# Optimization experiments

Measured on AMD Instinct MI355X. Metric: run time of the kernel, lower is better.

The kernel has to match this reference:

```python
import jax, jax.numpy as jnp
import numpy as np

B, D, L, H, HD, FF, WS, P = 64, 768, 12, 12, 64, 3072, 14, 16
N = WS * WS + 1  # 197 tokens (cls + 196 patches)
NRD = (2 * WS - 1) ** 2 + 3  # 732 relative distances
SCALE = HD ** -0.5


def _rel_index():
    coords = np.stack(np.meshgrid(np.arange(WS), np.arange(WS), indexing='ij')).reshape(2, -1)
    rel = (coords[:, :, None] - coords[:, None, :]).transpose(1, 2, 0)
    rel[..., 0] += WS - 1
    rel[..., 1] += WS - 1
    rel[..., 0] *= 2 * WS - 1
    idx = np.zeros((N, N), np.int32)
    idx[1:, 1:] = rel.sum(-1)
    idx[0, :] = NRD - 3
    idx[:, 0] = NRD - 2
    idx[0, 0] = NRD - 1
    return jnp.asarray(idx)

REL_IDX = _rel_index()


def setup_inputs() -> dict:
    key = jax.random.key(0)
    ks = jax.random.split(key, 12)
    rn = lambda k, shp: jax.random.normal(k, shp, jnp.float32) * 0.02
    return dict(
        x=jax.random.normal(ks[0], (B, 3, 224, 224), jnp.float32),
        patch_w=rn(ks[1], (D, 3 * P * P)),
        patch_b=jnp.zeros((D,), jnp.float32),
        cls_token=rn(ks[2], (1, 1, D)),
        pos_embed=rn(ks[3], (1, N, D)),
        ln1_w=jnp.ones((L, D), jnp.float32), ln1_b=jnp.zeros((L, D), jnp.float32),
        qkv_w=rn(ks[4], (L, 3 * D, D)),
        q_bias=jnp.zeros((L, D), jnp.float32), v_bias=jnp.zeros((L, D), jnp.float32),
        proj_w=rn(ks[5], (L, D, D)), proj_b=jnp.zeros((L, D), jnp.float32),
        ln2_w=jnp.ones((L, D), jnp.float32), ln2_b=jnp.zeros((L, D), jnp.float32),
        fc1_w=rn(ks[6], (L, FF, D)), fc1_b=jnp.zeros((L, FF), jnp.float32),
        fc2_w=rn(ks[7], (L, D, FF)), fc2_b=jnp.zeros((L, D), jnp.float32),
        gamma1=jnp.full((L, D), 0.1, jnp.float32), gamma2=jnp.full((L, D), 0.1, jnp.float32),
        rpb_table=rn(ks[8], (L, NRD, H)),
        fc_norm_w=jnp.ones((D,), jnp.float32), fc_norm_b=jnp.zeros((D,), jnp.float32),
    )


def _ln(x, w, b):
    mu = x.mean(-1, keepdims=True)
    var = ((x - mu) ** 2).mean(-1, keepdims=True)
    return (x - mu) * jax.lax.rsqrt(var + 1e-5) * w + b


def reference(x, patch_w, patch_b, cls_token, pos_embed, ln1_w, ln1_b, qkv_w, q_bias, v_bias,
              proj_w, proj_b, ln2_w, ln2_b, fc1_w, fc1_b, fc2_w, fc2_b, gamma1, gamma2,
              rpb_table, fc_norm_w, fc_norm_b):
    # Patch embed (Conv2d stride=kernel == patch extraction + matmul): [B,3,224,224] -> [B,196,D]
    p = x.reshape(B, 3, WS, P, WS, P).transpose(0, 2, 4, 1, 3, 5).reshape(B, WS * WS, 3 * P * P)
    t = p @ patch_w.T + patch_b
    t = jnp.concatenate([jnp.broadcast_to(cls_token, (B, 1, D)), t], axis=1) + pos_embed
    for l in range(L):
        h = _ln(t, ln1_w[l], ln1_b[l])
        qkvb = jnp.concatenate([q_bias[l], jnp.zeros((D,), t.dtype), v_bias[l]])
        qkv = (h @ qkv_w[l].T + qkvb).reshape(B, N, 3, H, HD).transpose(2, 0, 3, 1, 4)
        q, k, v = qkv[0] * SCALE, qkv[1], qkv[2]
        attn = jnp.einsum('bhnd,bhmd->bhnm', q, k)  # [B,H,N,N]
        bias = rpb_table[l][REL_IDX]  # [N,N,H] gathered relative-position bias
        attn = jax.nn.softmax(attn + bias.transpose(2, 0, 1)[None], axis=-1)
        o = jnp.einsum('bhnm,bhmd->bhnd', attn, v).transpose(0, 2, 1, 3).reshape(B, N, D)
        t = t + gamma1[l] * (o @ proj_w[l].T + proj_b[l])
        h = _ln(t, ln2_w[l], ln2_b[l])
        h = jax.nn.gelu(h @ fc1_w[l].T + fc1_b[l], approximate=False) @ fc2_w[l].T + fc2_b[l]
        t = t + gamma2[l] * h
    feat = t[:, 1:].mean(axis=1)  # mean-pool patch tokens (use_mean_pooling)
    return _ln(feat, fc_norm_w, fc_norm_b)
```

## Files before the change

### kernel.cpp

```cpp
#include <hip/hip_runtime.h>
#include <hip/hip_bf16.h>

typedef short bf16x8 __attribute__((ext_vector_type(8)));
typedef float f32x4 __attribute__((ext_vector_type(4)));

constexpr int D_  = 768;
constexpr int FF_ = 3072;
constexpr int HH  = 12;
constexpr int NT_ = 197;
constexpr int BB  = 64;
constexpr int BR  = BB * NT_;
constexpr int MP  = 12800;
constexpr int SN  = 224;
constexpr float SCALE_ = 0.125f;

#define MFMA16(a, b, c) __builtin_amdgcn_mfma_f32_16x16x32_bf16((a), (b), (c), 0, 0, 0)

__device__ __forceinline__ void gload_lds16(const __hip_bfloat16* g, __hip_bfloat16* l) {
  __builtin_amdgcn_global_load_lds((const __attribute__((address_space(1))) void*)g,
                                   (__attribute__((address_space(3))) void*)l, 16, 0, 0);
}


__global__ void patch_build(const float* __restrict__ x, __hip_bfloat16* __restrict__ p) {
  int e = blockIdx.x * 256 + threadIdx.x;
  int idx4 = e * 4;
  int col = idx4 % 768; int m = idx4 / 768;
  int c = col >> 8; int pi = (col >> 4) & 15; int pj = col & 15;
  int b = m / 196; int s = m - b * 196; int wi = s / 14; int wj = s - wi * 14;
  const float* src = x + (((size_t)b * 3 + c) * 224 + wi * 16 + pi) * 224 + wj * 16 + pj;
  float4 v = *(const float4*)src;
  __hip_bfloat16* dst = p + (size_t)idx4;
  dst[0] = __float2bfloat16(v.x);
  dst[1] = __float2bfloat16(v.y);
  dst[2] = __float2bfloat16(v.z);
  dst[3] = __float2bfloat16(v.w);
}

__global__ void cls_pos(const float* __restrict__ cls_tok, const float* __restrict__ pos, __hip_bfloat16* __restrict__ t) {
  int e = blockIdx.x * 256 + threadIdx.x;
  int b = e / 768, c = e - (e / 768) * 768;
  t[(size_t)(b * NT_) * D_ + c] = __float2bfloat16(cls_tok[c] + pos[c]);
}

__global__ void cvt_bf16(const float* __restrict__ in, __hip_bfloat16* __restrict__ out) {
  int e = blockIdx.x * 256 + threadIdx.x;
  float4 v = ((const float4*)in)[e];
  union { __hip_bfloat16 h[4]; short4 s4; } u;
  u.h[0] = __float2bfloat16(v.x); u.h[1] = __float2bfloat16(v.y);
  u.h[2] = __float2bfloat16(v.z); u.h[3] = __float2bfloat16(v.w);
  ((short4*)out)[e] = u.s4;
}

__global__ void cvt_layer(const float* __restrict__ qkv, const float* __restrict__ proj,
                          const float* __restrict__ fc1, const float* __restrict__ fc2,
                          __hip_bfloat16* __restrict__ wq, __hip_bfloat16* __restrict__ wp,
                          __hip_bfloat16* __restrict__ w1, __hip_bfloat16* __restrict__ w2) {
  int e = blockIdx.x * 256 + threadIdx.x;
  const float* src; __hip_bfloat16* dst;
  if (e < 442368)       { src = qkv; dst = wq; }
  else if (e < 589824)  { src = proj; dst = wp; e -= 442368; }
  else if (e < 1179648) { src = fc1;  dst = w1; e -= 589824; }
  else                  { src = fc2;  dst = w2; e -= 1179648; }
  float4 v = ((const float4*)src)[e];
  union { __hip_bfloat16 h[4]; short4 s4; } u;
  u.h[0] = __float2bfloat16(v.x); u.h[1] = __float2bfloat16(v.y);
  u.h[2] = __float2bfloat16(v.z); u.h[3] = __float2bfloat16(v.w);
  ((short4*)dst)[e] = u.s4;
}

__global__ void build_bias(const float* __restrict__ rpb, __hip_bfloat16* __restrict__ bias_all) {
  int e = blockIdx.x * 256 + threadIdx.x;
  int j = e % SN; int rest = e / SN; int i = rest % SN; int l = rest / SN;
  int idx;
  if (i >= 197 || j >= 197) idx = 0;
  else if (i == 0 && j == 0) idx = 731;
  else if (i == 0) idx = 729;
  else if (j == 0) idx = 730;
  else {
    int pi = i - 1, pj = j - 1;
    int ri = pi / 14, ci = pi - ri * 14, rj = pj / 14, cj = pj - rj * 14;
    idx = (ri - rj + 13) * 27 + (ci - cj + 13);
  }
  const float* src = rpb + ((size_t)l * 732 + idx) * HH;
  __hip_bfloat16* dst = bias_all + ((size_t)l * HH * SN + i) * SN + j;
  #pragma unroll
  for (int h = 0; h < HH; ++h) dst[(size_t)h * SN * SN] = __float2bfloat16(src[h]);
}

__global__ __launch_bounds__(256) void transp_v(const __hip_bfloat16* __restrict__ vb,
                                                __hip_bfloat16* __restrict__ vtb) {
  int bh = blockIdx.x;
  __shared__ unsigned short V_lds[SN][65];
  const unsigned short* src = (const unsigned short*)(vb + (size_t)bh * SN * 64);
  unsigned short* dst = (unsigned short*)(vtb + (size_t)bh * 64 * SN);
  int tid = threadIdx.x;
  #pragma unroll
  for (int c = 0; c < 14; ++c) {
    int id = c * 256 + tid;
    int e = id * 4;
    int nn = e >> 6, d = e & 63;
    ushort4 v = ((const ushort4*)src)[id];
    V_lds[nn][d] = v.x; V_lds[nn][d + 1] = v.y; V_lds[nn][d + 2] = v.z; V_lds[nn][d + 3] = v.w;
  }
  __syncthreads();
  #pragma unroll
  for (int c = 0; c < 14; ++c) {
    int id = c * 256 + tid;
    int e = id * 4;
    int d = e / SN, nn = e - d * SN;
    ushort4 v;
    v.x = V_lds[nn][d]; v.y = V_lds[nn + 1][d]; v.z = V_lds[nn + 2][d]; v.w = V_lds[nn + 3][d];
    ((ushort4*)dst)[id] = v;
  }
}

__device__ __forceinline__ void block_reduce2(float& s, float& q, int tid) {
  #pragma unroll
  for (int d = 32; d >= 1; d >>= 1) { s += __shfl_xor(s, d); q += __shfl_xor(q, d); }
  __shared__ float ss[4], qq[4];
  int wave = tid >> 6, lane = tid & 63;
  if (lane == 0) { ss[wave] = s; qq[wave] = q; }
  __syncthreads();
  s = ss[0] + ss[1] + ss[2] + ss[3];
  q = qq[0] + qq[1] + qq[2] + qq[3];
}

__global__ __launch_bounds__(256) void ln_rows(const __hip_bfloat16* __restrict__ t, const float* __restrict__ w,
                                               const float* __restrict__ b, __hip_bfloat16* __restrict__ out) {
  int row = blockIdx.x; int tid = threadIdx.x;
  const __hip_bfloat16* x = t + (size_t)row * D_;
  float v0 = __bfloat162float(x[tid]);
  float v1 = __bfloat162float(x[tid + 256]);
  float v2 = __bfloat162float(x[tid + 512]);
  float s = v0 + v1 + v2;
  float q = v0 * v0 + v1 * v1 + v2 * v2;
  block_reduce2(s, q, tid);
  float mu = s * (1.0f / 768.0f);
  float var = q * (1.0f / 768.0f) - mu * mu;
  float rs = rsqrtf(var + 1e-5f);
  __hip_bfloat16* o = out + (size_t)row * D_;
  o[tid]       = __float2bfloat16((v0 - mu) * rs * w[tid]       + b[tid]);
  o[tid + 256] = __float2bfloat16((v1 - mu) * rs * w[tid + 256] + b[tid + 256]);
  o[tid + 512] = __float2bfloat16((v2 - mu) * rs * w[tid + 512] + b[tid + 512]);
}

__global__ __launch_bounds__(256) void pool_ln(const __hip_bfloat16* __restrict__ t, const float* __restrict__ w,
                                               const float* __restrict__ b, float* __restrict__ out) {
  int bimg = blockIdx.x; int tid = threadIdx.x;
  const __hip_bfloat16* base = t + ((size_t)bimg * NT_ + 1) * D_;
  float a0 = 0.f, a1 = 0.f, a2 = 0.f;
  for (int s = 0; s < 196; ++s) {
    const __hip_bfloat16* r = base + (size_t)s * D_;
    a0 += __bfloat162float(r[tid]);
    a1 += __bfloat162float(r[tid + 256]);
    a2 += __bfloat162float(r[tid + 512]);
  }
  a0 *= (1.0f / 196.0f); a1 *= (1.0f / 196.0f); a2 *= (1.0f / 196.0f);
  float s = a0 + a1 + a2;
  float q = a0 * a0 + a1 * a1 + a2 * a2;
  block_reduce2(s, q, tid);
  float mu = s * (1.0f / 768.0f);
  float var = q * (1.0f / 768.0f) - mu * mu;
  float rs = rsqrtf(var + 1e-5f);
  float* o = out + (size_t)bimg * D_;
  o[tid]       = (a0 - mu) * rs * w[tid]       + b[tid];
  o[tid + 256] = (a1 - mu) * rs * w[tid + 256] + b[tid + 256];
  o[tid + 512] = (a2 - mu) * rs * w[tid + 512] + b[tid + 512];
}


enum { EPI_PATCH = 0, EPI_QKV = 1, EPI_GELU = 2, EPI_RESID = 3 };

struct GemmArgs {
  const __hip_bfloat16* A;
  const __hip_bfloat16* W;
  int K;
  int NTILES;
  const float* bias;
  const float* bias2;
  const float* gamma;
  const float* pos;
  __hip_bfloat16* tout;
  __hip_bfloat16* out;
  __hip_bfloat16* qo;
  __hip_bfloat16* ko;
  __hip_bfloat16* vo;
};

template <int MODE, int BM_>
__device__ __forceinline__ void gemm_body(GemmArgs p) {
  static_assert(BM_ == 128 || BM_ == 64, "");
  constexpr int MREP = BM_ / 32;
  const int tid = threadIdx.x, lane = tid & 63, wave = tid >> 6;
  const int wr = wave >> 1, wc = wave & 1;
  const int l15 = lane & 15, l4 = lane >> 4;
  const int K = p.K;

  const int nwg = gridDim.x;
  const int q = nwg >> 3, rm = nwg & 7;
  const int xcd = blockIdx.x & 7, sub = blockIdx.x >> 3;
  const int swb = (xcd < rm ? xcd * (q + 1) : rm * (q + 1) + (xcd - rm) * q) + sub;
  const int bn = swb % p.NTILES, bm = swb / p.NTILES;

  __shared__ __align__(16) __hip_bfloat16 As[BM_ * 64];
  __shared__ __align__(16) __hip_bfloat16 Bs[128 * 64];

  const int sr = tid >> 3, sc = tid & 7;
  const int swz = (sc ^ (sr & 7)) * 8;
  const __hip_bfloat16* a0 = p.A + (size_t)(bm * BM_ + sr) * K + swz;
  const __hip_bfloat16* b0 = p.W + (size_t)(bn * 128 + sr) * K + swz;
  const int ldsoff = wave * 512;

  auto stage = [&](int t) {
    #pragma unroll
    for (int i = 0; i < BM_ / 32; ++i)
      gload_lds16(a0 + (size_t)(i * 32) * K + (size_t)t * 64, &As[i * 2048 + ldsoff]);
    #pragma unroll
    for (int i = 0; i < 4; ++i)
      gload_lds16(b0 + (size_t)(i * 32) * K + (size_t)t * 64, &Bs[i * 2048 + ldsoff]);
  };
  auto rdA = [&](int m, int ks) {
    int row = wr * (BM_ / 2) + m * 16 + l15;
    return *(const bf16x8*)&As[row * 64 + (((ks << 2) + l4) ^ (row & 7)) * 8];
  };
  auto rdB = [&](int n, int ks) {
    int row = wc * 64 + n * 16 + l15;
    return *(const bf16x8*)&Bs[row * 64 + (((ks << 2) + l4) ^ (row & 7)) * 8];
  };

  f32x4 acc[MREP][4] = {};
  const int NKT = K >> 6;
  for (int t = 0; t < NKT; ++t) {
    if (t) asm volatile("s_barrier" ::: "memory");
    stage(t);
    asm volatile("s_waitcnt vmcnt(0)" ::: "memory");
    asm volatile("s_barrier" ::: "memory");
    #pragma unroll
    for (int ks = 0; ks < 2; ++ks) {
      bf16x8 af[MREP], bfr[4];
      #pragma unroll
      for (int m = 0; m < MREP; ++m) af[m] = rdA(m, ks);
      #pragma unroll
      for (int n = 0; n < 4; ++n) bfr[n] = rdB(n, ks);
      #pragma unroll
      for (int m = 0; m < MREP; ++m)
        #pragma unroll
        for (int n = 0; n < 4; ++n)
          acc[m][n] = MFMA16(af[m], bfr[n], acc[m][n]);
    }
  }

  const int mb = bm * BM_ + wr * (BM_ / 2);
  const int nbase = bn * 128 + wc * 64;
  if constexpr (MODE == EPI_QKV) {
    #pragma unroll
    for (int j = 0; j < 4; ++j) {
      const int n = nbase + j * 16 + l15;
      const int which = n / D_, d = n - which * D_;
      const int head = d >> 6, hd = d & 63;
      #pragma unroll
      for (int i = 0; i < MREP; ++i) {
        #pragma unroll
        for (int rr = 0; rr < 4; ++rr) {
          const int m = mb + i * 16 + l4 * 4 + rr;
          if (m < BR) {
            const int b = m / NT_, nn = m - (m / NT_) * NT_;
            float v = acc[i][j][rr];
            if (which == 0)
              p.qo[(((size_t)(b * HH + head)) * SN + nn) * 64 + hd] = __float2bfloat16((v + p.bias[d]) * SCALE_);
            else if (which == 1)
              p.ko[(((size_t)(b * HH + head)) * SN + nn) * 64 + hd] = __float2bfloat16(v);
            else
              p.vo[(((size_t)(b * HH + head)) * SN + nn) * 64 + hd] = __float2bfloat16(v + p.bias2[d]);
          }
        }
      }
    }
  } else {
    #pragma unroll
    for (int i = 0; i < MREP; ++i) {
      #pragma unroll
      for (int rr = 0; rr < 4; ++rr) {
        const int m = mb + i * 16 + l4 * 4 + rr;
        if constexpr (MODE == EPI_PATCH) {
          const int b = m / 196, s = m - (m / 196) * 196;
          __hip_bfloat16* dst = p.tout + ((size_t)(b * NT_ + s + 1)) * D_;
          const float* pose = p.pos + (size_t)(s + 1) * D_;
          #pragma unroll
          for (int j = 0; j < 4; ++j) {
            int n = nbase + j * 16 + l15;
            dst[n] = __float2bfloat16(acc[i][j][rr] + p.bias[n] + pose[n]);
          }
        } else if constexpr (MODE == EPI_GELU) {
          __hip_bfloat16* dst = p.out + (size_t)m * FF_;
          #pragma unroll
          for (int j = 0; j < 4; ++j) {
            int n = nbase + j * 16 + l15;
            float u = acc[i][j][rr] + p.bias[n];
            float z = 1.59576912f * (u + 0.044715f * u * u * u);
            float g = u * (1.0f / (1.0f + __expf(-z)));
            dst[n] = __float2bfloat16(g);
          }
        } else {
          if (m < BR) {
            __hip_bfloat16* dst = p.tout + (size_t)m * D_;
            #pragma unroll
            for (int j = 0; j < 4; ++j) {
              int n = nbase + j * 16 + l15;
              float old = __bfloat162float(dst[n]);
              dst[n] = __float2bfloat16(old + p.gamma[n] * (acc[i][j][rr] + p.bias[n]));
            }
          }
        }
      }
    }
  }
}

__global__ __launch_bounds__(256, 4) void gA_patch(GemmArgs p) { gemm_body<EPI_PATCH, 128>(p); }
__global__ __launch_bounds__(256, 4) void gB_qkv(GemmArgs p)   { gemm_body<EPI_QKV, 128>(p); }
__global__ __launch_bounds__(256, 4) void gC_proj(GemmArgs p)  { gemm_body<EPI_RESID, 64>(p); }
__global__ __launch_bounds__(256, 4) void gD_fc1(GemmArgs p)   { gemm_body<EPI_GELU, 128>(p); }
__global__ __launch_bounds__(256, 4) void gE_fc2(GemmArgs p)   { gemm_body<EPI_RESID, 64>(p); }


__global__ __launch_bounds__(256) void attn_kernel(const __hip_bfloat16* __restrict__ qb,
    const __hip_bfloat16* __restrict__ kb, const __hip_bfloat16* __restrict__ vtb,
    const __hip_bfloat16* __restrict__ biasL, __hip_bfloat16* __restrict__ o) {
  int bh = blockIdx.x; int b = bh / HH, h = bh - b * HH;
  int lane = threadIdx.x & 63, wave = threadIdx.x >> 6;
  int l15 = lane & 15, l4 = lane >> 4;
  __shared__ __align__(16) __hip_bfloat16 probs[4][16][SN];
  const __hip_bfloat16* Q  = qb  + (size_t)bh * SN * 64;
  const __hip_bfloat16* Kp = kb  + (size_t)bh * SN * 64;
  const __hip_bfloat16* VT = vtb + (size_t)bh * 64 * SN;
  const __hip_bfloat16* BIAS = biasL + (size_t)h * SN * SN;
  for (int mt = wave; mt < 13; mt += 4) {
    int m0 = mt * 16;
    bf16x8 qf0 = *(const bf16x8*)(Q + ((size_t)(m0 + l15)) * 64 + l4 * 8);
    bf16x8 qf1 = *(const bf16x8*)(Q + ((size_t)(m0 + l15)) * 64 + 32 + l4 * 8);
    f32x4 sc[14] = {};
    #pragma unroll
    for (int nt = 0; nt < 14; ++nt) {
      bf16x8 kf0 = *(const bf16x8*)(Kp + ((size_t)(nt * 16 + l15)) * 64 + l4 * 8);
      bf16x8 kf1 = *(const bf16x8*)(Kp + ((size_t)(nt * 16 + l15)) * 64 + 32 + l4 * 8);
      sc[nt] = __builtin_amdgcn_mfma_f32_16x16x32_bf16(qf0, kf0, sc[nt], 0, 0, 0);
      sc[nt] = __builtin_amdgcn_mfma_f32_16x16x32_bf16(qf1, kf1, sc[nt], 0, 0, 0);
    }
    float rmax[4] = {-1e30f, -1e30f, -1e30f, -1e30f};
    #pragma unroll
    for (int nt = 0; nt < 14; ++nt) {
      int j = nt * 16 + l15;
      #pragma unroll
      for (int r = 0; r < 4; ++r) {
        int i = m0 + l4 * 4 + r;
        float v = (j < 197) ? (sc[nt][r] + __bfloat162float(BIAS[i * SN + j])) : -1e30f;
        sc[nt][r] = v;
        rmax[r] = fmaxf(rmax[r], v);
      }
    }
    #pragma unroll
    for (int r = 0; r < 4; ++r)
      #pragma unroll
      for (int d = 1; d < 16; d <<= 1)
        rmax[r] = fmaxf(rmax[r], __shfl_xor(rmax[r], d));
    float rsum[4] = {0.f, 0.f, 0.f, 0.f};
    #pragma unroll
    for (int nt = 0; nt < 14; ++nt)
      #pragma unroll
      for (int r = 0; r < 4; ++r) {
        float e = __expf(sc[nt][r] - rmax[r]);
        sc[nt][r] = e;
        rsum[r] += e;
      }
    #pragma unroll
    for (int r = 0; r < 4; ++r) {
      #pragma unroll
      for (int d = 1; d < 16; d <<= 1) rsum[r] += __shfl_xor(rsum[r], d);
      rsum[r] = 1.0f / rsum[r];
    }
    #pragma unroll
    for (int nt = 0; nt < 14; ++nt)
      #pragma unroll
      for (int r = 0; r < 4; ++r)
        probs[wave][l4 * 4 + r][nt * 16 + l15] = __float2bfloat16(sc[nt][r] * rsum[r]);
    asm volatile("s_waitcnt lgkmcnt(0)" ::: "memory");
    __builtin_amdgcn_sched_barrier(0);
    f32x4 oc[4] = {};
    #pragma unroll
    for (int kt = 0; kt < 7; ++kt) {
      bf16x8 pf = *(const bf16x8*)&probs[wave][l15][kt * 32 + l4 * 8];
      #pragma unroll
      for (int nt = 0; nt < 4; ++nt) {
        bf16x8 vf = *(const bf16x8*)(VT + ((size_t)(nt * 16 + l15)) * SN + kt * 32 + l4 * 8);
        oc[nt] = __builtin_amdgcn_mfma_f32_16x16x32_bf16(pf, vf, oc[nt], 0, 0, 0);
      }
    }
    #pragma unroll
    for (int nt = 0; nt < 4; ++nt)
      #pragma unroll
      for (int r = 0; r < 4; ++r) {
        int i = m0 + l4 * 4 + r;
        if (i < 197)
          o[((size_t)(b * NT_ + i)) * D_ + h * 64 + nt * 16 + l15] = __float2bfloat16(oc[nt][r]);
      }
  }
}


extern "C" void kernel_launch(void* const* d_in, const int* in_sizes, int n_in,
                              void* d_out, int out_size, void* d_ws, size_t ws_size,
                              hipStream_t stream) {
  const float* x       = (const float*)d_in[0];
  const float* patch_w = (const float*)d_in[1];
  const float* patch_b = (const float*)d_in[2];
  const float* cls_tok = (const float*)d_in[3];
  const float* pos_emb = (const float*)d_in[4];
  const float* ln1_w   = (const float*)d_in[5];
  const float* ln1_b   = (const float*)d_in[6];
  const float* qkv_w   = (const float*)d_in[7];
  const float* q_bias  = (const float*)d_in[8];
  const float* v_bias  = (const float*)d_in[9];
  const float* proj_w  = (const float*)d_in[10];
  const float* proj_b  = (const float*)d_in[11];
  const float* ln2_w   = (const float*)d_in[12];
  const float* ln2_b   = (const float*)d_in[13];
  const float* fc1_w   = (const float*)d_in[14];
  const float* fc1_b   = (const float*)d_in[15];
  const float* fc2_w   = (const float*)d_in[16];
  const float* fc2_b   = (const float*)d_in[17];
  const float* gamma1  = (const float*)d_in[18];
  const float* gamma2  = (const float*)d_in[19];
  const float* rpb     = (const float*)d_in[20];
  const float* fcn_w   = (const float*)d_in[21];
  const float* fcn_b   = (const float*)d_in[22];
  float* out = (float*)d_out;

  char* ws = (char*)d_ws;
  size_t off = 0;
  auto alloc = [&](size_t bytes) -> void* {
    void* p = ws + off;
    off = (off + bytes + 255) & ~(size_t)255;
    return p;
  };
  __hip_bfloat16* t   = (__hip_bfloat16*)alloc((size_t)MP * D_ * 2);
  __hip_bfloat16* h   = (__hip_bfloat16*)alloc((size_t)MP * D_ * 2);
  __hip_bfloat16* ob  = (__hip_bfloat16*)alloc((size_t)MP * D_ * 2);
  __hip_bfloat16* mid = (__hip_bfloat16*)alloc((size_t)MP * FF_ * 2);
  __hip_bfloat16* qb  = (__hip_bfloat16*)alloc((size_t)BB * HH * SN * 64 * 2);
  __hip_bfloat16* kb  = (__hip_bfloat16*)alloc((size_t)BB * HH * SN * 64 * 2);
  __hip_bfloat16* vb  = (__hip_bfloat16*)alloc((size_t)BB * HH * SN * 64 * 2);
  __hip_bfloat16* vtb = (__hip_bfloat16*)alloc((size_t)BB * HH * 64 * SN * 2);
  __hip_bfloat16* bias_all = (__hip_bfloat16*)alloc((size_t)12 * HH * SN * SN * 2);
  __hip_bfloat16* wq  = (__hip_bfloat16*)alloc((size_t)2304 * 768 * 2);
  __hip_bfloat16* wp  = (__hip_bfloat16*)alloc((size_t)768 * 768 * 2);
  __hip_bfloat16* w1  = (__hip_bfloat16*)alloc((size_t)3072 * 768 * 2);
  __hip_bfloat16* w2  = (__hip_bfloat16*)alloc((size_t)768 * 3072 * 2);
  __hip_bfloat16* wpt = (__hip_bfloat16*)alloc((size_t)768 * 768 * 2);

  patch_build<<<9408, 256, 0, stream>>>(x, mid);
  cvt_bf16<<<576, 256, 0, stream>>>(patch_w, wpt);
  cls_pos<<<192, 256, 0, stream>>>(cls_tok, pos_emb, t);
  build_bias<<<2352, 256, 0, stream>>>(rpb, bias_all);
  {
    GemmArgs g = {};
    g.A = mid; g.W = wpt; g.K = 768; g.NTILES = 6;
    g.bias = patch_b; g.pos = pos_emb; g.tout = t;
    gA_patch<<<98 * 6, 256, 0, stream>>>(g);
  }
  for (int l = 0; l < 12; ++l) {
    cvt_layer<<<6912, 256, 0, stream>>>(qkv_w + (size_t)l * 2304 * 768, proj_w + (size_t)l * 768 * 768,
                                        fc1_w + (size_t)l * 3072 * 768, fc2_w + (size_t)l * 768 * 3072,
                                        wq, wp, w1, w2);
    ln_rows<<<BR, 256, 0, stream>>>(t, ln1_w + l * 768, ln1_b + l * 768, h);
    {
      GemmArgs g = {};
      g.A = h; g.W = wq; g.K = 768; g.NTILES = 18;
      g.bias = q_bias + l * 768; g.bias2 = v_bias + l * 768;
      g.qo = qb; g.ko = kb; g.vo = vb;
      gB_qkv<<<100 * 18, 256, 0, stream>>>(g);
    }
    transp_v<<<768, 256, 0, stream>>>(vb, vtb);
    attn_kernel<<<768, 256, 0, stream>>>(qb, kb, vtb, bias_all + (size_t)l * HH * SN * SN, ob);
    {
      GemmArgs g = {};
      g.A = ob; g.W = wp; g.K = 768; g.NTILES = 6;
      g.bias = proj_b + l * 768; g.gamma = gamma1 + l * 768; g.tout = t;
      gC_proj<<<200 * 6, 256, 0, stream>>>(g);
    }
    ln_rows<<<BR, 256, 0, stream>>>(t, ln2_w + l * 768, ln2_b + l * 768, h);
    {
      GemmArgs g = {};
      g.A = h; g.W = w1; g.K = 768; g.NTILES = 24;
      g.bias = fc1_b + l * 3072; g.out = mid;
      gD_fc1<<<100 * 24, 256, 0, stream>>>(g);
    }
    {
      GemmArgs g = {};
      g.A = mid; g.W = w2; g.K = 3072; g.NTILES = 6;
      g.bias = fc2_b + l * 768; g.gamma = gamma2 + l * 768; g.tout = t;
      gE_fc2<<<200 * 6, 256, 0, stream>>>(g);
    }
  }
  pool_ln<<<64, 256, 0, stream>>>(t, fcn_w, fcn_b, out);
}
```

Baseline: 4.850 ms.

## Double-buffer GEMM LDS tiles with K=32 steps to overlap loads and MFMA

Changes the GEMM mainloop from a single 64-wide K tile that was loaded and then computed to two 32-wide K buffers in LDS. The next tile is prefetched via global_load_lds while the current one is computed, using partial vmcnt waits. The swizzle is adapted to the 32-column layout. The cost is twice as many barriers per K element and fewer MFMAs per iteration, and correctness relies on the hand-counted vmcnt values.

```diff
diff --git a/kernel.cpp b/kernel.cpp
--- a/kernel.cpp
+++ b/kernel.cpp
@@ -192,6 +192,8 @@
 __device__ __forceinline__ void gemm_body(GemmArgs p) {
   static_assert(BM_ == 128 || BM_ == 64, "");
   constexpr int MREP = BM_ / 32;
+  constexpr int AISS = BM_ / 64;
+  constexpr int NVM  = AISS + 2;
   const int tid = threadIdx.x, lane = tid & 63, wave = tid >> 6;
   const int wr = wave >> 1, wc = wave & 1;
   const int l15 = lane & 15, l4 = lane >> 4;
@@ -203,52 +205,56 @@
   const int swb = (xcd < rm ? xcd * (q + 1) : rm * (q + 1) + (xcd - rm) * q) + sub;
   const int bn = swb % p.NTILES, bm = swb / p.NTILES;
 
-  __shared__ __align__(16) __hip_bfloat16 As[BM_ * 64];
-  __shared__ __align__(16) __hip_bfloat16 Bs[128 * 64];
-
-  const int sr = tid >> 3, sc = tid & 7;
-  const int swz = (sc ^ (sr & 7)) * 8;
+  __shared__ __align__(16) __hip_bfloat16 As[2][BM_ * 32];
+  __shared__ __align__(16) __hip_bfloat16 Bs[2][128 * 32];
+
+  const int sr = tid >> 2, sc = tid & 3;
+  const int swz = (sc ^ ((sr >> 1) & 3)) * 8;
   const __hip_bfloat16* a0 = p.A + (size_t)(bm * BM_ + sr) * K + swz;
   const __hip_bfloat16* b0 = p.W + (size_t)(bn * 128 + sr) * K + swz;
   const int ldsoff = wave * 512;
 
-  auto stage = [&](int t) {
-    #pragma unroll
-    for (int i = 0; i < BM_ / 32; ++i)
-      gload_lds16(a0 + (size_t)(i * 32) * K + (size_t)t * 64, &As[i * 2048 + ldsoff]);
-    #pragma unroll
-    for (int i = 0; i < 4; ++i)
-      gload_lds16(b0 + (size_t)(i * 32) * K + (size_t)t * 64, &Bs[i * 2048 + ldsoff]);
+  auto stage = [&](int t, int buf) {
+    #pragma unroll
+    for (int i = 0; i < AISS; ++i)
+      gload_lds16(a0 + (size_t)(i * 64) * K + (size_t)t * 32, &As[buf][i * 2048 + ldsoff]);
+    #pragma unroll
+    for (int i = 0; i < 2; ++i)
+      gload_lds16(b0 + (size_t)(i * 64) * K + (size_t)t * 32, &Bs[buf][i * 2048 + ldsoff]);
   };
-  auto rdA = [&](int m, int ks) {
+  auto rdA = [&](int buf, int m) {
     int row = wr * (BM_ / 2) + m * 16 + l15;
-    return *(const bf16x8*)&As[row * 64 + (((ks << 2) + l4) ^ (row & 7)) * 8];
+    return *(const bf16x8*)&As[buf][row * 32 + (l4 ^ ((row >> 1) & 3)) * 8];
   };
-  auto rdB = [&](int n, int ks) {
+  auto rdB = [&](int buf, int n) {
     int row = wc * 64 + n * 16 + l15;
-    return *(const bf16x8*)&Bs[row * 64 + (((ks << 2) + l4) ^ (row & 7)) * 8];
+    return *(const bf16x8*)&Bs[buf][row * 32 + (l4 ^ ((row >> 1) & 3)) * 8];
   };
 
   f32x4 acc[MREP][4] = {};
-  const int NKT = K >> 6;
+  const int NKT = K >> 5;
+  stage(0, 0);
   for (int t = 0; t < NKT; ++t) {
-    if (t) asm volatile("s_barrier" ::: "memory");
-    stage(t);
-    asm volatile("s_waitcnt vmcnt(0)" ::: "memory");
+    const int cur = t & 1;
+    if (t + 1 < NKT) {
+      stage(t + 1, cur ^ 1);
+      if constexpr (NVM == 4) asm volatile("s_waitcnt vmcnt(4)" ::: "memory");
+      else                    asm volatile("s_waitcnt vmcnt(3)" ::: "memory");
+    } else {
+      asm volatile("s_waitcnt vmcnt(0)" ::: "memory");
+    }
     asm volatile("s_barrier" ::: "memory");
-    #pragma unroll
-    for (int ks = 0; ks < 2; ++ks) {
-      bf16x8 af[MREP], bfr[4];
-      #pragma unroll
-      for (int m = 0; m < MREP; ++m) af[m] = rdA(m, ks);
-      #pragma unroll
-      for (int n = 0; n < 4; ++n) bfr[n] = rdB(n, ks);
-      #pragma unroll
-      for (int m = 0; m < MREP; ++m)
-        #pragma unroll
-        for (int n = 0; n < 4; ++n)
-          acc[m][n] = MFMA16(af[m], bfr[n], acc[m][n]);
-    }
+    bf16x8 af[MREP], bfr[4];
+    #pragma unroll
+    for (int m = 0; m < MREP; ++m) af[m] = rdA(cur, m);
+    #pragma unroll
+    for (int n = 0; n < 4; ++n) bfr[n] = rdB(cur, n);
+    #pragma unroll
+    for (int m = 0; m < MREP; ++m)
+      #pragma unroll
+      for (int n = 0; n < 4; ++n)
+        acc[m][n] = MFMA16(af[m], bfr[n], acc[m][n]);
+    asm volatile("s_barrier" ::: "memory");
   }
 
   const int mb = bm * BM_ + wr * (BM_ / 2);
```

Measured after the change: 5.517 ms. +13.8%, slower.
